# Kernel optimization log

Measured on AMD Instinct MI355X. Metric: run time of the kernel, lower is better.

Reference implementation:

```python
import jax, jax.numpy as jnp
import numpy as np

N_CHANNELS = 8
SECTION = 32768
F_IN = 64
F_OUT = 64
UNITS = 512


def setup_inputs() -> dict:
    key = jax.random.key(0)
    ks = jax.random.split(key, 10)
    scale = lambda fan_in: 1.0 / np.sqrt(fan_in)
    return {
        "x": jax.random.normal(ks[0], (N_CHANNELS * SECTION, F_IN), jnp.float32),
        "w0": jax.random.normal(ks[1], (N_CHANNELS, UNITS, F_IN), jnp.float32) * scale(F_IN),
        "w1": jax.random.normal(ks[2], (N_CHANNELS, UNITS, UNITS), jnp.float32) * scale(UNITS),
        "w2": jax.random.normal(ks[3], (N_CHANNELS, UNITS, UNITS), jnp.float32) * scale(UNITS),
        "w3": jax.random.normal(ks[4], (N_CHANNELS, F_OUT, UNITS), jnp.float32) * scale(UNITS),
        "b0": jax.random.normal(ks[5], (N_CHANNELS, UNITS), jnp.float32) * 0.01,
        "b1": jax.random.normal(ks[6], (N_CHANNELS, UNITS), jnp.float32) * 0.01,
        "b2": jax.random.normal(ks[7], (N_CHANNELS, UNITS), jnp.float32) * 0.01,
        "b3": jax.random.normal(ks[8], (N_CHANNELS, F_OUT), jnp.float32) * 0.01,
        "section_size": SECTION,
    }


def reference(x, w0, w1, w2, w3, b0, b1, b2, b3, section_size):
    # Equal sections of size `section_size` per channel: reshape to [C, S, F]
    # and run the per-channel MLP as batched (grouped) GEMMs.
    C = w0.shape[0]
    xs = x.reshape(C, section_size, -1)  # [C, S, F_in]
    for w, b in ((w0, b0), (w1, b1), (w2, b2)):
        xs = jax.nn.relu(jnp.einsum('csi,coi->cso', xs, w) + b[:, None, :])
    ys = jnp.einsum('csi,coi->cso', xs, w3) + b3[:, None, :]  # [C, S, F_out]
    return ys.reshape(C * section_size, -1)
```

## Files before the change

kernel.cpp:

```cpp
#include <hip/hip_runtime.h>
#include <hip/hip_bf16.h>

#define CH 8
#define SEC 32768
#define FIN 64
#define FOUT 64
#define UN 512
#define BM 128

typedef __bf16 bf16;
typedef bf16 bf16x8 __attribute__((ext_vector_type(8)));
typedef bf16 bf16x4 __attribute__((ext_vector_type(4)));
typedef float f32x4 __attribute__((ext_vector_type(4)));

__device__ __forceinline__ bf16x8 cvt8(const float* __restrict__ src) {
  f32x4 u0 = *(const f32x4*)src;
  f32x4 u1 = *(const f32x4*)(src + 4);
  bf16x8 v;
  v[0] = (bf16)u0[0]; v[1] = (bf16)u0[1]; v[2] = (bf16)u0[2]; v[3] = (bf16)u0[3];
  v[4] = (bf16)u1[0]; v[5] = (bf16)u1[1]; v[6] = (bf16)u1[2]; v[7] = (bf16)u1[3];
  return v;
}

__device__ __forceinline__ void store_cvt8(void* dst, const float* __restrict__ src) {
  *(bf16x8*)dst = cvt8(src);
}

template<int K, bool WSPATH>
__device__ __forceinline__ void run_main_layer(
    const bf16* __restrict__ wb,
    const float* __restrict__ wf,
    const float* __restrict__ bias, char* __restrict__ act,
    int w, int l, int l15, int l4, int wm, int wn)
{
  constexpr int NKS = K / 32;
  const int col0 = wn * 128;
  const char* abase = act + wm * (4 * NKS * 1024) + l * 16;

  f32x4 acc[4][8];
#pragma unroll
  for (int mt = 0; mt < 4; ++mt)
#pragma unroll
    for (int nt = 0; nt < 8; ++nt)
      acc[mt][nt] = f32x4{0.f, 0.f, 0.f, 0.f};

  if constexpr (WSPATH) {
    const bf16* bp = wb + ((size_t)(wn * 8) * NKS * 64 + l) * 8;
    bf16x8 B0[8], B1[8];
#pragma unroll
    for (int i = 0; i < 8; ++i)
      B0[i] = *(const bf16x8*)(bp + (size_t)(i * NKS) * 512);

#pragma unroll
    for (int j = 0; j < NKS; j += 2) {
      if (j + 1 < NKS) {
#pragma unroll
        for (int i = 0; i < 8; ++i)
          B1[i] = *(const bf16x8*)(bp + (size_t)(i * NKS + j + 1) * 512);
      }
      {
        bf16x8 a[4];
#pragma unroll
        for (int mt = 0; mt < 4; ++mt)
          a[mt] = *(const bf16x8*)(abase + (mt * NKS + j) * 1024);
        __builtin_amdgcn_s_setprio(1);
#pragma unroll
        for (int mt = 0; mt < 4; ++mt)
#pragma unroll
          for (int nt = 0; nt < 8; ++nt)
            acc[mt][nt] = __builtin_amdgcn_mfma_f32_16x16x32_bf16(B0[nt], a[mt], acc[mt][nt], 0, 0, 0);
        __builtin_amdgcn_s_setprio(0);
      }
      if (j + 2 < NKS) {
#pragma unroll
        for (int i = 0; i < 8; ++i)
          B0[i] = *(const bf16x8*)(bp + (size_t)(i * NKS + j + 2) * 512);
      }
      if (j + 1 < NKS) {
        bf16x8 a[4];
#pragma unroll
        for (int mt = 0; mt < 4; ++mt)
          a[mt] = *(const bf16x8*)(abase + (mt * NKS + j + 1) * 1024);
        __builtin_amdgcn_s_setprio(1);
#pragma unroll
        for (int mt = 0; mt < 4; ++mt)
#pragma unroll
          for (int nt = 0; nt < 8; ++nt)
            acc[mt][nt] = __builtin_amdgcn_mfma_f32_16x16x32_bf16(B1[nt], a[mt], acc[mt][nt], 0, 0, 0);
        __builtin_amdgcn_s_setprio(0);
      }
    }
  } else {
    const float* bpf[8];
#pragma unroll
    for (int nt = 0; nt < 8; ++nt)
      bpf[nt] = wf + (size_t)(col0 + nt * 16 + l15) * K + l4 * 8;
#pragma unroll
    for (int j = 0; j < NKS; ++j) {
      bf16x8 a[4], b[8];
#pragma unroll
      for (int nt = 0; nt < 8; ++nt) b[nt] = cvt8(bpf[nt] + j * 32);
#pragma unroll
      for (int mt = 0; mt < 4; ++mt)
        a[mt] = *(const bf16x8*)(abase + (mt * NKS + j) * 1024);
#pragma unroll
      for (int mt = 0; mt < 4; ++mt)
#pragma unroll
        for (int nt = 0; nt < 8; ++nt)
          acc[mt][nt] = __builtin_amdgcn_mfma_f32_16x16x32_bf16(b[nt], a[mt], acc[mt][nt], 0, 0, 0);
    }
  }

  __syncthreads();

#pragma unroll
  for (int nt = 0; nt < 8; ++nt) {
    const f32x4 bv = *(const f32x4*)(bias + col0 + nt * 16 + l4 * 4);
    const int slot = l15 + ((nt & 1) * 2 + (l4 >> 1)) * 16;
    const int ksp  = wn * 4 + (nt >> 1);
    const int boff = slot * 16 + (l4 & 1) * 8;
#pragma unroll
    for (int mt = 0; mt < 4; ++mt) {
      bf16x4 pk;
#pragma unroll
      for (int r = 0; r < 4; ++r) {
        const float v = acc[mt][nt][r] + bv[r];
        pk[r] = (bf16)(v > 0.f ? v : 0.f);
      }
      *(bf16x4*)(act + ((wm * 4 + mt) * 16 + ksp) * 1024 + boff) = pk;
    }
  }
  __syncthreads();
}

template<bool WSPATH>
__device__ __forceinline__ void run_final_layer(
    const bf16* __restrict__ wb, const float* __restrict__ wf,
    const float* __restrict__ bias, const char* __restrict__ act,
    float* __restrict__ gout,
    int w, int l, int l15, int l4)
{
  constexpr int NKS = 16;
  const char* abase = act + w * (NKS * 1024) + l * 16;

  f32x4 acc[4];
#pragma unroll
  for (int f = 0; f < 4; ++f) acc[f] = f32x4{0.f, 0.f, 0.f, 0.f};

  if constexpr (WSPATH) {
    const bf16* bp = wb + (size_t)l * 8;
    bf16x8 B0[4], B1[4];
#pragma unroll
    for (int f = 0; f < 4; ++f)
      B0[f] = *(const bf16x8*)(bp + (size_t)(f * NKS) * 512);
#pragma unroll
    for (int j = 0; j < NKS; j += 2) {
      {
#pragma unroll
        for (int f = 0; f < 4; ++f)
          B1[f] = *(const bf16x8*)(bp + (size_t)(f * NKS + j + 1) * 512);
        const bf16x8 a = *(const bf16x8*)(abase + j * 1024);
#pragma unroll
        for (int f = 0; f < 4; ++f)
          acc[f] = __builtin_amdgcn_mfma_f32_16x16x32_bf16(B0[f], a, acc[f], 0, 0, 0);
      }
      {
        if (j + 2 < NKS) {
#pragma unroll
          for (int f = 0; f < 4; ++f)
            B0[f] = *(const bf16x8*)(bp + (size_t)(f * NKS + j + 2) * 512);
        }
        const bf16x8 a = *(const bf16x8*)(abase + (j + 1) * 1024);
#pragma unroll
        for (int f = 0; f < 4; ++f)
          acc[f] = __builtin_amdgcn_mfma_f32_16x16x32_bf16(B1[f], a, acc[f], 0, 0, 0);
      }
    }
  } else {
    const float* bpf[4];
#pragma unroll
    for (int f = 0; f < 4; ++f)
      bpf[f] = wf + (size_t)(f * 16 + l15) * UN + l4 * 8;
#pragma unroll
    for (int j = 0; j < NKS; ++j) {
      const bf16x8 a = *(const bf16x8*)(abase + j * 1024);
#pragma unroll
      for (int f = 0; f < 4; ++f) {
        const bf16x8 b = cvt8(bpf[f] + j * 32);
        acc[f] = __builtin_amdgcn_mfma_f32_16x16x32_bf16(b, a, acc[f], 0, 0, 0);
      }
    }
  }

#pragma unroll
  for (int f = 0; f < 4; ++f) {
    const f32x4 bv = *(const f32x4*)(bias + f * 16 + l4 * 4);
    f32x4 o;
#pragma unroll
    for (int r = 0; r < 4; ++r) o[r] = acc[f][r] + bv[r];
    *(f32x4*)(gout + (size_t)(w * 16 + l15) * FOUT + f * 16 + l4 * 4) = o;
  }
}

template<bool WSPATH>
__global__ __launch_bounds__(512, 2) void mlp_fused(
    const float* __restrict__ x,
    const float* __restrict__ w0f, const float* __restrict__ w1f,
    const float* __restrict__ w2f, const float* __restrict__ w3f,
    const float* __restrict__ b0, const float* __restrict__ b1,
    const float* __restrict__ b2, const float* __restrict__ b3,
    const bf16* __restrict__ wbase,
    float* __restrict__ out)
{
  extern __shared__ char smem[];
  char* act = smem;

  const int tid = threadIdx.x;
  const int w = tid >> 6, l = tid & 63;
  const int l15 = l & 15, l4 = l >> 4;
  const int wm = w >> 2, wn = w & 3;

  const int wg = (blockIdx.x & 7) * 256 + (blockIdx.x >> 3);
  const int ch = wg >> 8;
  const int row0 = (wg & 255) * BM;

  const bf16* w0b = wbase + (size_t)ch * UN * FIN;
  const bf16* w1b = wbase + CH * UN * FIN + (size_t)ch * UN * UN;
  const bf16* w2b = wbase + CH * UN * FIN + CH * UN * UN + (size_t)ch * UN * UN;
  const bf16* w3b = wbase + CH * UN * FIN + 2 * CH * UN * UN + (size_t)ch * FOUT * UN;
  const float* w0c = w0f + (size_t)ch * UN * FIN;
  const float* w1c = w1f + (size_t)ch * UN * UN;
  const float* w2c = w2f + (size_t)ch * UN * UN;
  const float* w3c = w3f + (size_t)ch * FOUT * UN;
  const float* b0c = b0 + ch * UN;
  const float* b1c = b1 + ch * UN;
  const float* b2c = b2 + ch * UN;
  const float* b3c = b3 + ch * FOUT;

  {
    const float* xs = x + (size_t)(ch * SEC + row0) * FIN;
#pragma unroll
    for (int i = 0; i < 2; ++i) {
      const int s = w * 2 + i;
      store_cvt8(act + s * 1024 + l * 16,
                 xs + ((s >> 1) * 16 + l15) * FIN + (s & 1) * 32 + l4 * 8);
    }
  }
  __syncthreads();

  run_main_layer<64,  WSPATH>(w0b, w0c, b0c, act, w, l, l15, l4, wm, wn);
  run_main_layer<512, WSPATH>(w1b, w1c, b1c, act, w, l, l15, l4, wm, wn);
  run_main_layer<512, WSPATH>(w2b, w2c, b2c, act, w, l, l15, l4, wm, wn);
  run_final_layer<WSPATH>(w3b, w3c, b3c, act,
                          out + (size_t)(ch * SEC + row0) * FOUT,
                          w, l, l15, l4);
}

template<int K, int N>
__device__ __forceinline__ void cvt_one(const float* __restrict__ src,
                                        bf16* __restrict__ dst, int t)
{
  constexpr int NKS = K / 32;
  constexpr int perCh = N * K / 8;
  const int ch = t / perCh;
  const int r = t - ch * perCh;
  const int l = r & 63;
  const int p = r >> 6;
  const int ks = p & (NKS - 1);
  const int f = p / NKS;
  const float* s = src + (size_t)ch * N * K + (size_t)(f * 16 + (l & 15)) * K
                 + ks * 32 + (l >> 4) * 8;
  store_cvt8(dst + (size_t)t * 8, s);
}

__global__ void cvt_weights(const float* __restrict__ w0, const float* __restrict__ w1,
                            const float* __restrict__ w2, const float* __restrict__ w3,
                            bf16* __restrict__ o)
{
  constexpr int T0 = CH * UN * FIN / 8;
  constexpr int T1 = CH * UN * UN / 8;
  constexpr int total = 2 * T0 + 2 * T1;
  for (int t = blockIdx.x * blockDim.x + threadIdx.x; t < total;
       t += gridDim.x * blockDim.x) {
    if (t < T0)                cvt_one<FIN, UN>(w0, o, t);
    else if (t < T0 + T1)      cvt_one<UN, UN>(w1, o + CH * UN * FIN, t - T0);
    else if (t < T0 + 2 * T1)  cvt_one<UN, UN>(w2, o + CH * UN * FIN + CH * UN * UN, t - T0 - T1);
    else                       cvt_one<UN, FOUT>(w3, o + CH * UN * FIN + 2 * CH * UN * UN, t - T0 - 2 * T1);
  }
}

extern "C" void kernel_launch(void* const* d_in, const int* in_sizes, int n_in,
                              void* d_out, int out_size, void* d_ws, size_t ws_size,
                              hipStream_t stream)
{
  const float* x  = (const float*)d_in[0];
  const float* w0 = (const float*)d_in[1];
  const float* w1 = (const float*)d_in[2];
  const float* w2 = (const float*)d_in[3];
  const float* w3 = (const float*)d_in[4];
  const float* b0 = (const float*)d_in[5];
  const float* b1 = (const float*)d_in[6];
  const float* b2 = (const float*)d_in[7];
  const float* b3 = (const float*)d_in[8];
  float* out = (float*)d_out;

  const int grid = CH * (SEC / BM);
  const size_t wbytes = (size_t)(2 * CH * UN * FIN + 2 * CH * UN * UN) * 2;

  if (ws_size >= wbytes) {
    bf16* wb = (bf16*)d_ws;
    hipLaunchKernelGGL(cvt_weights, dim3(2304), dim3(256), 0, stream, w0, w1, w2, w3, wb);
    hipFuncSetAttribute(reinterpret_cast<const void*>(mlp_fused<true>),
                        hipFuncAttributeMaxDynamicSharedMemorySize, 131072);
    hipLaunchKernelGGL(mlp_fused<true>, dim3(grid), dim3(512), 131072, stream,
                       x, w0, w1, w2, w3, b0, b1, b2, b3, wb, out);
  } else {
    hipFuncSetAttribute(reinterpret_cast<const void*>(mlp_fused<false>),
                        hipFuncAttributeMaxDynamicSharedMemorySize, 131072);
    hipLaunchKernelGGL(mlp_fused<false>, dim3(grid), dim3(512), 131072, stream,
                       x, w0, w1, w2, w3, b0, b1, b2, b3, (const bf16*)nullptr, out);
  }
}
```

Before: 299.3 us.

## Switch fused MLP to 32x32x16 MFMA tiles with per-wave column split

Replaces the 16x16x32 bf16 MFMA tiling with 32x32x16 MFMA instructions. Each of the 8 waves now owns a 64-column slice across all 128 rows instead of a 2x4 wave grid. The activation LDS layout, weight pre-swizzle, input staging and final layer are all reworked to match the 32-row fragment layout, and A fragments are now double-buffered alongside B. The aim is fewer, larger MFMA issues and less per-wave B fetch traffic. The cost is that every wave reads the full activation tile from LDS, which raises LDS read pressure.

```diff
diff --git a/kernel.cpp b/kernel.cpp
--- a/kernel.cpp
+++ b/kernel.cpp
@@ -12,6 +12,7 @@
 typedef bf16 bf16x8 __attribute__((ext_vector_type(8)));
 typedef bf16 bf16x4 __attribute__((ext_vector_type(4)));
 typedef float f32x4 __attribute__((ext_vector_type(4)));
+typedef float f32x16 __attribute__((ext_vector_type(16)));
 
 __device__ __forceinline__ bf16x8 cvt8(const float* __restrict__ src) {
   f32x4 u0 = *(const f32x4*)src;
@@ -31,103 +32,107 @@
     const bf16* __restrict__ wb,
     const float* __restrict__ wf,
     const float* __restrict__ bias, char* __restrict__ act,
-    int w, int l, int l15, int l4, int wm, int wn)
-{
-  constexpr int NKS = K / 32;
-  const int col0 = wn * 128;
-  const char* abase = act + wm * (4 * NKS * 1024) + l * 16;
-
-  f32x4 acc[4][8];
+    int w, int l, int l31, int hi)
+{
+  constexpr int NKS = K / 16;
+  const int col0 = w * 64;
+  const char* abase = act + l * 16;
+
+  f32x16 acc[4][2];
 #pragma unroll
   for (int mt = 0; mt < 4; ++mt)
 #pragma unroll
-    for (int nt = 0; nt < 8; ++nt)
-      acc[mt][nt] = f32x4{0.f, 0.f, 0.f, 0.f};
+    for (int nt = 0; nt < 2; ++nt)
+#pragma unroll
+      for (int r = 0; r < 16; ++r) acc[mt][nt][r] = 0.f;
 
   if constexpr (WSPATH) {
-    const bf16* bp = wb + ((size_t)(wn * 8) * NKS * 64 + l) * 8;
-    bf16x8 B0[8], B1[8];
-#pragma unroll
-    for (int i = 0; i < 8; ++i)
+    const bf16* bp = wb + ((size_t)(w * 2) * NKS * 64 + l) * 8;
+    bf16x8 B0[2], B1[2], A0[4], A1[4];
+#pragma unroll
+    for (int i = 0; i < 2; ++i)
       B0[i] = *(const bf16x8*)(bp + (size_t)(i * NKS) * 512);
+#pragma unroll
+    for (int mt = 0; mt < 4; ++mt)
+      A0[mt] = *(const bf16x8*)(abase + (mt * NKS) * 1024);
 
 #pragma unroll
     for (int j = 0; j < NKS; j += 2) {
+      {
+        if (j + 1 < NKS) {
+#pragma unroll
+          for (int i = 0; i < 2; ++i)
+            B1[i] = *(const bf16x8*)(bp + (size_t)(i * NKS + j + 1) * 512);
+#pragma unroll
+          for (int mt = 0; mt < 4; ++mt)
+            A1[mt] = *(const bf16x8*)(abase + (mt * NKS + j + 1) * 1024);
+        }
+        __builtin_amdgcn_s_setprio(1);
+#pragma unroll
+        for (int mt = 0; mt < 4; ++mt)
+#pragma unroll
+          for (int nt = 0; nt < 2; ++nt)
+            acc[mt][nt] = __builtin_amdgcn_mfma_f32_32x32x16_bf16(B0[nt], A0[mt], acc[mt][nt], 0, 0, 0);
+        __builtin_amdgcn_s_setprio(0);
+      }
       if (j + 1 < NKS) {
-#pragma unroll
-        for (int i = 0; i < 8; ++i)
-          B1[i] = *(const bf16x8*)(bp + (size_t)(i * NKS + j + 1) * 512);
-      }
-      {
-        bf16x8 a[4];
+        if (j + 2 < NKS) {
+#pragma unroll
+          for (int i = 0; i < 2; ++i)
+            B0[i] = *(const bf16x8*)(bp + (size_t)(i * NKS + j + 2) * 512);
+#pragma unroll
+          for (int mt = 0; mt < 4; ++mt)
+            A0[mt] = *(const bf16x8*)(abase + (mt * NKS + j + 2) * 1024);
+        }
+        __builtin_amdgcn_s_setprio(1);
 #pragma unroll
         for (int mt = 0; mt < 4; ++mt)
-          a[mt] = *(const bf16x8*)(abase + (mt * NKS + j) * 1024);
-        __builtin_amdgcn_s_setprio(1);
-#pragma unroll
-        for (int mt = 0; mt < 4; ++mt)
-#pragma unroll
-          for (int nt = 0; nt < 8; ++nt)
-            acc[mt][nt] = __builtin_amdgcn_mfma_f32_16x16x32_bf16(B0[nt], a[mt], acc[mt][nt], 0, 0, 0);
+#pragma unroll
+          for (int nt = 0; nt < 2; ++nt)
+            acc[mt][nt] = __builtin_amdgcn_mfma_f32_32x32x16_bf16(B1[nt], A1[mt], acc[mt][nt], 0, 0, 0);
         __builtin_amdgcn_s_setprio(0);
       }
-      if (j + 2 < NKS) {
-#pragma unroll
-        for (int i = 0; i < 8; ++i)
-          B0[i] = *(const bf16x8*)(bp + (size_t)(i * NKS + j + 2) * 512);
-      }
-      if (j + 1 < NKS) {
-        bf16x8 a[4];
-#pragma unroll
-        for (int mt = 0; mt < 4; ++mt)
-          a[mt] = *(const bf16x8*)(abase + (mt * NKS + j + 1) * 1024);
-        __builtin_amdgcn_s_setprio(1);
-#pragma unroll
-        for (int mt = 0; mt < 4; ++mt)
-#pragma unroll
-          for (int nt = 0; nt < 8; ++nt)
-            acc[mt][nt] = __builtin_amdgcn_mfma_f32_16x16x32_bf16(B1[nt], a[mt], acc[mt][nt], 0, 0, 0);
-        __builtin_amdgcn_s_setprio(0);
-      }
     }
   } else {
-    const float* bpf[8];
-#pragma unroll
-    for (int nt = 0; nt < 8; ++nt)
-      bpf[nt] = wf + (size_t)(col0 + nt * 16 + l15) * K + l4 * 8;
+    const float* bpf[2];
+#pragma unroll
+    for (int nt = 0; nt < 2; ++nt)
+      bpf[nt] = wf + (size_t)(col0 + nt * 32 + l31) * K + hi * 8;
 #pragma unroll
     for (int j = 0; j < NKS; ++j) {
-      bf16x8 a[4], b[8];
-#pragma unroll
-      for (int nt = 0; nt < 8; ++nt) b[nt] = cvt8(bpf[nt] + j * 32);
+      bf16x8 a[4], b[2];
+#pragma unroll
+      for (int nt = 0; nt < 2; ++nt) b[nt] = cvt8(bpf[nt] + j * 16);
 #pragma unroll
       for (int mt = 0; mt < 4; ++mt)
         a[mt] = *(const bf16x8*)(abase + (mt * NKS + j) * 1024);
 #pragma unroll
       for (int mt = 0; mt < 4; ++mt)
 #pragma unroll
-        for (int nt = 0; nt < 8; ++nt)
-          acc[mt][nt] = __builtin_amdgcn_mfma_f32_16x16x32_bf16(b[nt], a[mt], acc[mt][nt], 0, 0, 0);
+        for (int nt = 0; nt < 2; ++nt)
+          acc[mt][nt] = __builtin_amdgcn_mfma_f32_32x32x16_bf16(b[nt], a[mt], acc[mt][nt], 0, 0, 0);
     }
   }
 
   __syncthreads();
 
 #pragma unroll
-  for (int nt = 0; nt < 8; ++nt) {
-    const f32x4 bv = *(const f32x4*)(bias + col0 + nt * 16 + l4 * 4);
-    const int slot = l15 + ((nt & 1) * 2 + (l4 >> 1)) * 16;
-    const int ksp  = wn * 4 + (nt >> 1);
-    const int boff = slot * 16 + (l4 & 1) * 8;
-#pragma unroll
-    for (int mt = 0; mt < 4; ++mt) {
-      bf16x4 pk;
-#pragma unroll
-      for (int r = 0; r < 4; ++r) {
-        const float v = acc[mt][nt][r] + bv[r];
-        pk[r] = (bf16)(v > 0.f ? v : 0.f);
-      }
-      *(bf16x4*)(act + ((wm * 4 + mt) * 16 + ksp) * 1024 + boff) = pk;
+  for (int nt = 0; nt < 2; ++nt) {
+#pragma unroll
+    for (int q = 0; q < 4; ++q) {
+      const f32x4 bv = *(const f32x4*)(bias + col0 + nt * 32 + q * 8 + hi * 4);
+      const int ksp  = (col0 >> 4) + nt * 2 + (q >> 1);
+      const int boff = ((q & 1) * 32 + l31) * 16 + hi * 8;
+#pragma unroll
+      for (int mt = 0; mt < 4; ++mt) {
+        bf16x4 pk;
+#pragma unroll
+        for (int r = 0; r < 4; ++r) {
+          const float v = acc[mt][nt][q * 4 + r] + bv[r];
+          pk[r] = (bf16)(v > 0.f ? v : 0.f);
+        }
+        *(bf16x4*)(act + (mt * 32 + ksp) * 1024 + boff) = pk;
+      }
     }
   }
   __syncthreads();
@@ -138,67 +143,52 @@
     const bf16* __restrict__ wb, const float* __restrict__ wf,
     const float* __restrict__ bias, const char* __restrict__ act,
     float* __restrict__ gout,
-    int w, int l, int l15, int l4)
-{
-  constexpr int NKS = 16;
-  const char* abase = act + w * (NKS * 1024) + l * 16;
-
-  f32x4 acc[4];
-#pragma unroll
-  for (int f = 0; f < 4; ++f) acc[f] = f32x4{0.f, 0.f, 0.f, 0.f};
+    int w, int l, int l31, int hi)
+{
+  constexpr int NKS = 32;
+  const int tm = w >> 1, tn = w & 1;
+  const char* abase = act + tm * (NKS * 1024) + l * 16;
+
+  f32x16 acc;
+#pragma unroll
+  for (int r = 0; r < 16; ++r) acc[r] = 0.f;
 
   if constexpr (WSPATH) {
-    const bf16* bp = wb + (size_t)l * 8;
-    bf16x8 B0[4], B1[4];
-#pragma unroll
-    for (int f = 0; f < 4; ++f)
-      B0[f] = *(const bf16x8*)(bp + (size_t)(f * NKS) * 512);
+    const bf16* bp = wb + ((size_t)tn * NKS * 64 + l) * 8;
+    bf16x8 B0 = *(const bf16x8*)(bp), B1;
+    bf16x8 A0 = *(const bf16x8*)(abase), A1;
 #pragma unroll
     for (int j = 0; j < NKS; j += 2) {
       {
-#pragma unroll
-        for (int f = 0; f < 4; ++f)
-          B1[f] = *(const bf16x8*)(bp + (size_t)(f * NKS + j + 1) * 512);
-        const bf16x8 a = *(const bf16x8*)(abase + j * 1024);
-#pragma unroll
-        for (int f = 0; f < 4; ++f)
-          acc[f] = __builtin_amdgcn_mfma_f32_16x16x32_bf16(B0[f], a, acc[f], 0, 0, 0);
+        B1 = *(const bf16x8*)(bp + (size_t)(j + 1) * 512);
+        A1 = *(const bf16x8*)(abase + (j + 1) * 1024);
+        acc = __builtin_amdgcn_mfma_f32_32x32x16_bf16(B0, A0, acc, 0, 0, 0);
       }
       {
         if (j + 2 < NKS) {
-#pragma unroll
-          for (int f = 0; f < 4; ++f)
-            B0[f] = *(const bf16x8*)(bp + (size_t)(f * NKS + j + 2) * 512);
+          B0 = *(const bf16x8*)(bp + (size_t)(j + 2) * 512);
+          A0 = *(const bf16x8*)(abase + (j + 2) * 1024);
         }
-        const bf16x8 a = *(const bf16x8*)(abase + (j + 1) * 1024);
-#pragma unroll
-        for (int f = 0; f < 4; ++f)
-          acc[f] = __builtin_amdgcn_mfma_f32_16x16x32_bf16(B1[f], a, acc[f], 0, 0, 0);
+        acc = __builtin_amdgcn_mfma_f32_32x32x16_bf16(B1, A1, acc, 0, 0, 0);
       }
     }
   } else {
-    const float* bpf[4];
-#pragma unroll
-    for (int f = 0; f < 4; ++f)
-      bpf[f] = wf + (size_t)(f * 16 + l15) * UN + l4 * 8;
+    const float* bpf = wf + (size_t)(tn * 32 + l31) * UN + hi * 8;
 #pragma unroll
     for (int j = 0; j < NKS; ++j) {
+      const bf16x8 b = cvt8(bpf + j * 16);
       const bf16x8 a = *(const bf16x8*)(abase + j * 1024);
-#pragma unroll
-      for (int f = 0; f < 4; ++f) {
-        const bf16x8 b = cvt8(bpf[f] + j * 32);
-        acc[f] = __builtin_amdgcn_mfma_f32_16x16x32_bf16(b, a, acc[f], 0, 0, 0);
-      }
-    }
-  }
-
-#pragma unroll
-  for (int f = 0; f < 4; ++f) {
-    const f32x4 bv = *(const f32x4*)(bias + f * 16 + l4 * 4);
+      acc = __builtin_amdgcn_mfma_f32_32x32x16_bf16(b, a, acc, 0, 0, 0);
+    }
+  }
+
+#pragma unroll
+  for (int q = 0; q < 4; ++q) {
+    const f32x4 bv = *(const f32x4*)(bias + tn * 32 + q * 8 + hi * 4);
     f32x4 o;
 #pragma unroll
-    for (int r = 0; r < 4; ++r) o[r] = acc[f][r] + bv[r];
-    *(f32x4*)(gout + (size_t)(w * 16 + l15) * FOUT + f * 16 + l4 * 4) = o;
+    for (int r = 0; r < 4; ++r) o[r] = acc[q * 4 + r] + bv[r];
+    *(f32x4*)(gout + (size_t)(tm * 32 + l31) * FOUT + tn * 32 + q * 8 + hi * 4) = o;
   }
 }
 
@@ -217,8 +207,7 @@
 
   const int tid = threadIdx.x;
   const int w = tid >> 6, l = tid & 63;
-  const int l15 = l & 15, l4 = l >> 4;
-  const int wm = w >> 2, wn = w & 3;
+  const int l31 = l & 31, hi = l >> 5;
 
   const int wg = (blockIdx.x & 7) * 256 + (blockIdx.x >> 3);
   const int ch = wg >> 8;
@@ -242,25 +231,26 @@
 #pragma unroll
     for (int i = 0; i < 2; ++i) {
       const int s = w * 2 + i;
+      const int mt = s >> 2, ks = s & 3;
       store_cvt8(act + s * 1024 + l * 16,
-                 xs + ((s >> 1) * 16 + l15) * FIN + (s & 1) * 32 + l4 * 8);
+                 xs + (size_t)(mt * 32 + l31) * FIN + ks * 16 + hi * 8);
     }
   }
   __syncthreads();
 
-  run_main_layer<64,  WSPATH>(w0b, w0c, b0c, act, w, l, l15, l4, wm, wn);
-  run_main_layer<512, WSPATH>(w1b, w1c, b1c, act, w, l, l15, l4, wm, wn);
-  run_main_layer<512, WSPATH>(w2b, w2c, b2c, act, w, l, l15, l4, wm, wn);
+  run_main_layer<64,  WSPATH>(w0b, w0c, b0c, act, w, l, l31, hi);
+  run_main_layer<512, WSPATH>(w1b, w1c, b1c, act, w, l, l31, hi);
+  run_main_layer<512, WSPATH>(w2b, w2c, b2c, act, w, l, l31, hi);
   run_final_layer<WSPATH>(w3b, w3c, b3c, act,
                           out + (size_t)(ch * SEC + row0) * FOUT,
-                          w, l, l15, l4);
+                          w, l, l31, hi);
 }
 
 template<int K, int N>
 __device__ __forceinline__ void cvt_one(const float* __restrict__ src,
                                         bf16* __restrict__ dst, int t)
 {
-  constexpr int NKS = K / 32;
+  constexpr int NKS = K / 16;
   constexpr int perCh = N * K / 8;
   const int ch = t / perCh;
   const int r = t - ch * perCh;
@@ -268,8 +258,8 @@
   const int p = r >> 6;
   const int ks = p & (NKS - 1);
   const int f = p / NKS;
-  const float* s = src + (size_t)ch * N * K + (size_t)(f * 16 + (l & 15)) * K
-                 + ks * 32 + (l >> 4) * 8;
+  const float* s = src + (size_t)ch * N * K + (size_t)(f * 32 + (l & 31)) * K
+                 + ks * 16 + (l >> 5) * 8;
   store_cvt8(dst + (size_t)t * 8, s);
 }
 
```

After: 293.3 us. 2.0% less time.
